# Kernel optimization log

Measured on AMD Instinct MI355X. Metric: run time of the kernel, lower is better.

## Reference

```python
import jax, jax.numpy as jnp
import numpy as np

B, N, E = 8, 512, 65536          # graphs per batch, nodes per graph, total edges
D_IN, D_H = 128, 64              # psi_1 in/out channels
R_IN, R_OUT = 32, 32             # psi_2 in/out channels (rnd indicator dim)
STEPS = 2                        # num consensus steps
NT = B * N                       # total nodes


def _gnn(x, src, dst, ea, W_root, W_nbr, b):
    """Edge-weighted GraphConv: relu(x W_root + A_w x W_nbr + b)."""
    msg = x[src] * ea                                    # [E, F] gather + scale
    agg = jax.ops.segment_sum(msg, dst, num_segments=NT)  # scatter-add
    return jax.nn.relu(x @ W_root + agg @ W_nbr + b)


def setup_inputs() -> dict:
    key = jax.random.key(0)
    ks = jax.random.split(key, 16)
    off = jnp.repeat(jnp.arange(B, dtype=jnp.int32) * N, E // B)  # keep edges within graphs

    def edges(k):
        k1, k2 = jax.random.split(k)
        src = jax.random.randint(k1, (E,), 0, N) + off
        dst = jax.random.randint(k2, (E,), 0, N) + off
        return jnp.stack([src, dst]).astype(jnp.int32)

    s = 0.1
    inp = {
        "x_s": jax.random.normal(ks[0], (NT, D_IN), jnp.float32),
        "edge_index_s": edges(ks[1]),
        "edge_attr_s": jax.random.uniform(ks[2], (E, 1), jnp.float32),
        "batch_s": jnp.repeat(jnp.arange(B, dtype=jnp.int32), N),
        "x_t": jax.random.normal(ks[3], (NT, D_IN), jnp.float32),
        "edge_index_t": edges(ks[4]),
        "edge_attr_t": jax.random.uniform(ks[5], (E, 1), jnp.float32),
        "batch_t": jnp.repeat(jnp.arange(B, dtype=jnp.int32), N),
        "r_s_all": jax.random.normal(ks[6], (STEPS, B, N, R_IN), jnp.float32),
        # psi_1 params
        "W1_root": jax.random.normal(ks[7], (D_IN, D_H), jnp.float32) * s,
        "W1_nbr": jax.random.normal(ks[8], (D_IN, D_H), jnp.float32) * s,
        "b1": jnp.zeros((D_H,), jnp.float32),
        # psi_2 params
        "W2_root": jax.random.normal(ks[9], (R_IN, R_OUT), jnp.float32) * s,
        "W2_nbr": jax.random.normal(ks[10], (R_IN, R_OUT), jnp.float32) * s,
        "b2": jnp.zeros((R_OUT,), jnp.float32),
        # consensus MLP: Lin(R_OUT,R_OUT) -> ReLU -> Lin(R_OUT,1)
        "Wm1": jax.random.normal(ks[11], (R_OUT, R_OUT), jnp.float32) * s,
        "bm1": jnp.zeros((R_OUT,), jnp.float32),
        "Wm2": jax.random.normal(ks[12], (R_OUT, 1), jnp.float32) * s,
        "bm2": jnp.zeros((1,), jnp.float32),
    }
    return inp


def reference(x_s, edge_index_s, edge_attr_s, batch_s,
              x_t, edge_index_t, edge_attr_t, batch_t, r_s_all,
              W1_root, W1_nbr, b1, W2_root, W2_nbr, b2,
              Wm1, bm1, Wm2, bm2):
    src_s, dst_s = edge_index_s[0], edge_index_s[1]
    src_t, dst_t = edge_index_t[0], edge_index_t[1]

    # psi_1: local matching embeddings
    h_s = _gnn(x_s, src_s, dst_s, edge_attr_s, W1_root, W1_nbr, b1)
    h_t = _gnn(x_t, src_t, dst_t, edge_attr_t, W1_root, W1_nbr, b1)

    # to_dense_batch: graphs are equal-sized (batch = repeat(arange(B), N)),
    # so dense batching is a reshape and all node masks are True ->
    # masked_softmax reduces to plain softmax (masked_fill is a no-op).
    h_s = h_s.reshape(B, N, D_H)
    h_t = h_t.reshape(B, N, D_H)

    S_hat0 = jnp.einsum('bsd,btd->bst', h_s, h_t)  # [B, N, N]
    S_0 = jax.nn.softmax(S_hat0, axis=-1)

    def mlp(D):  # D: [B, N, N, R_OUT] -> [B, N, N]
        h = jax.nn.relu(D @ Wm1 + bm1)
        return (h @ Wm2 + bm2)[..., 0]

    def step(S_hat, r_s):
        S = jax.nn.softmax(S_hat, axis=-1)
        r_t = jnp.einsum('bst,bsr->btr', S, r_s)        # S^T @ r_s
        o_s = _gnn(r_s.reshape(NT, R_IN), src_s, dst_s, edge_attr_s,
                   W2_root, W2_nbr, b2).reshape(B, N, R_OUT)
        o_t = _gnn(r_t.reshape(NT, R_IN), src_t, dst_t, edge_attr_t,
                   W2_root, W2_nbr, b2).reshape(B, N, R_OUT)
        D = o_s[:, :, None, :] - o_t[:, None, :, :]     # [B, N, N, R_OUT]
        return S_hat + mlp(D), None

    S_hat, _ = jax.lax.scan(step, S_hat0, r_s_all)
    S_L = jax.nn.softmax(S_hat, axis=-1)
    return (S_0, S_L)
```

## Files before the change

### kernel.cpp

```cpp
#include <hip/hip_runtime.h>

constexpr int B = 8, N = 512, E = 65536;
constexpr int D_IN = 128, D_H = 64, R_IN = 32, R_OUT = 32;
constexpr int NT = B * N;
constexpr size_t NN = (size_t)B * N * N;
constexpr int CAP = 64;

__global__ __launch_bounds__(256) void setup_pack(
    const int* __restrict__ src_s, const int* __restrict__ dst_s,
    const float* __restrict__ ea_s,
    const int* __restrict__ src_t, const int* __restrict__ dst_t,
    const float* __restrict__ ea_t,
    int* __restrict__ deg, int2* __restrict__ pack_s, int2* __restrict__ pack_t,
    const float* __restrict__ x_s, const float* __restrict__ x_t,
    const float* __restrict__ Wr, const float* __restrict__ Wn,
    const float* __restrict__ b,
    float* __restrict__ xr, float* __restrict__ xn) {
  __shared__ float smem[32 * D_IN + D_IN * 128];
  const int bid = blockIdx.x;
  const int tid = threadIdx.x;

  if (bid < 512) {
    const int gid = bid * 256 + tid;
    const int side = gid >> 16;
    const int e = gid & (E - 1);
    const int* __restrict__ src = side ? src_t : src_s;
    const int* __restrict__ dst = side ? dst_t : dst_s;
    const float* __restrict__ ea = side ? ea_t : ea_s;
    int2* __restrict__ pack = side ? pack_t : pack_s;
    const int d = dst[e];
    const int slot = atomicAdd(&deg[side * NT + d], 1);
    if (slot < CAP)
      pack[((size_t)d << 6) + slot] = make_int2(src[e], __float_as_int(ea[e]));
    return;
  }

  float (*xls)[D_IN] = (float(*)[D_IN])smem;
  float (*Wb)[128]   = (float(*)[128])(smem + 32 * D_IN);
  const int pb = bid - 512;
  const int side = pb >> 7;
  const int n0 = (pb & 127) * 32;
  const float* __restrict__ x = side ? x_t : x_s;

#pragma unroll
  for (int j = 0; j < 4; ++j) {
    const int i = tid + j * 256;
    const int n = i >> 5, k4 = (i & 31) * 4;
    *(float4*)&xls[n][k4] = *(const float4*)(x + (size_t)(n0 + n) * D_IN + k4);
  }
#pragma unroll
  for (int j = 0; j < 8; ++j) {
    const int i = tid + j * 256;
    const int k = i >> 4, c4 = (i & 15) * 4;
    *(float4*)&Wb[k][c4]      = *(const float4*)(Wr + k * D_H + c4);
    *(float4*)&Wb[k][64 + c4] = *(const float4*)(Wn + k * D_H + c4);
  }
  __syncthreads();

  const int c0 = (tid & 31) * 4;
  const int nb = (tid >> 5) * 4;
  float4 bv = make_float4(0.f, 0.f, 0.f, 0.f);
  if (c0 < 64) bv = *(const float4*)(b + c0);
  float4 acc0 = bv, acc1 = bv, acc2 = bv, acc3 = bv;

#pragma unroll 16
  for (int k = 0; k < D_IN; ++k) {
    const float4 w = *(const float4*)&Wb[k][c0];
    const float x0 = xls[nb + 0][k];
    const float x1 = xls[nb + 1][k];
    const float x2 = xls[nb + 2][k];
    const float x3 = xls[nb + 3][k];
    acc0.x += x0 * w.x; acc0.y += x0 * w.y; acc0.z += x0 * w.z; acc0.w += x0 * w.w;
    acc1.x += x1 * w.x; acc1.y += x1 * w.y; acc1.z += x1 * w.z; acc1.w += x1 * w.w;
    acc2.x += x2 * w.x; acc2.y += x2 * w.y; acc2.z += x2 * w.z; acc2.w += x2 * w.w;
    acc3.x += x3 * w.x; acc3.y += x3 * w.y; acc3.z += x3 * w.z; acc3.w += x3 * w.w;
  }

  const size_t gbase = (size_t)(side * NT + n0 + nb);
  if (c0 < 64) {
    *(float4*)(xr + (gbase + 0) * D_H + c0) = acc0;
    *(float4*)(xr + (gbase + 1) * D_H + c0) = acc1;
    *(float4*)(xr + (gbase + 2) * D_H + c0) = acc2;
    *(float4*)(xr + (gbase + 3) * D_H + c0) = acc3;
  } else {
    const int c = c0 - 64;
    *(float4*)(xn + (gbase + 0) * D_H + c) = acc0;
    *(float4*)(xn + (gbase + 1) * D_H + c) = acc1;
    *(float4*)(xn + (gbase + 2) * D_H + c) = acc2;
    *(float4*)(xn + (gbase + 3) * D_H + c) = acc3;
  }
}

__global__ __launch_bounds__(256) void agg_pack(
    const float* __restrict__ xn, const float* __restrict__ xr,
    const int* __restrict__ deg,
    const int2* __restrict__ pack_s, const int2* __restrict__ pack_t,
    float* __restrict__ h,
    const float* __restrict__ r_all,
    const float* __restrict__ W2r, const float* __restrict__ W2n,
    const float* __restrict__ b2,
    const float* __restrict__ Wm1, const float* __restrict__ bm1,
    float* __restrict__ Psb) {
  __shared__ float sh[3 * 8 * 33];
  const int bid = blockIdx.x;
  const int tid = threadIdx.x;

  if (bid < 512) {
    const int gid = bid * 256 + tid;
    const int side = gid >> 16;
    const int local = gid & 65535;
    const int n = local >> 4;
    const int c4 = (local & 15) * 4;
    const int2* __restrict__ pack = side ? pack_t : pack_s;
    const float* __restrict__ xb = xn + (size_t)side * NT * D_H;
    const int cnt = deg[side * NT + n];
    const size_t base = (size_t)n << 6;
    float4 acc = make_float4(0.f, 0.f, 0.f, 0.f);
    for (int k = 0; k < cnt; ++k) {
      const int2 p = pack[base + k];
      const float w = __int_as_float(p.y);
      const float4 v = *(const float4*)(xb + (size_t)p.x * D_H + c4);
      acc.x += v.x * w; acc.y += v.y * w; acc.z += v.z * w; acc.w += v.w * w;
    }
    const size_t oi = ((size_t)side * NT + n) * D_H + c4;
    const float4 rv = *(const float4*)(xr + oi);
    *(float4*)(h + oi) = make_float4(fmaxf(rv.x + acc.x, 0.f), fmaxf(rv.y + acc.y, 0.f),
                                     fmaxf(rv.z + acc.z, 0.f), fmaxf(rv.w + acc.w, 0.f));
    return;
  }

  float (*agg)[33] = (float(*)[33])sh;
  float (*rr)[33]  = (float(*)[33])(sh + 8 * 33);
  float (*o)[33]   = (float(*)[33])(sh + 16 * 33);
  const int blk = bid - 512;
  const int st = blk >> 9;
  const int n0 = (blk & 511) * 8;
  const float* __restrict__ r = r_all + (size_t)st * NT * R_IN;
  const int g = tid >> 5, j = tid & 31;
  const int n = n0 + g;
  const int cnt = deg[n];
  const size_t base = (size_t)n << 6;
  float acc = 0.f;
  for (int k = 0; k < cnt; ++k) {
    const int2 p = pack_s[base + k];
    acc += r[(size_t)p.x * R_IN + j] * __int_as_float(p.y);
  }
  agg[g][j] = acc;
  rr[g][j] = r[(size_t)n * R_IN + j];
  __syncthreads();
  float v = b2[j];
#pragma unroll 8
  for (int k = 0; k < 32; ++k)
    v += rr[g][k] * W2r[k * 32 + j] + agg[g][k] * W2n[k * 32 + j];
  o[g][j] = fmaxf(v, 0.f);
  __syncthreads();
  float p2 = bm1[j];
#pragma unroll 8
  for (int k = 0; k < 32; ++k) p2 += o[g][k] * Wm1[k * 32 + j];
  Psb[((size_t)st * NT + n) * 32 + j] = p2;
}

__global__ __launch_bounds__(512) void gemm_sm(const float* __restrict__ h,
                                               float* __restrict__ Shat,
                                               float* __restrict__ S0) {
  __shared__ float hs[16][65];
  __shared__ float ht[256][65];
  const int b = blockIdx.x >> 5;
  const int s0 = (blockIdx.x & 31) * 16;
  const int tid = threadIdx.x;
  const int sg = tid >> 6;
  const int tg = tid & 63;
  const float* __restrict__ h_t = h + (size_t)NT * D_H;

  if (tid < 256) {
    const int r = tid >> 4, c4 = (tid & 15) * 4;
    *(float4*)&hs[r][c4] =
        *(const float4*)(h + ((size_t)(b * N + s0 + r)) * D_H + c4);
  }

  float l[2][4][2];
#pragma unroll
  for (int ch = 0; ch < 2; ++ch) {
    __syncthreads();
#pragma unroll
    for (int jj = 0; jj < 8; ++jj) {
      const int i = tid + jj * 512;
      const int r = i >> 4, c4 = (i & 15) * 4;
      *(float4*)&ht[r][c4] =
          *(const float4*)(h_t + ((size_t)(b * N + ch * 256 + r)) * D_H + c4);
    }
    __syncthreads();
    float a[4][2];
#pragma unroll
    for (int j = 0; j < 4; ++j) { a[j][0] = 0.f; a[j][1] = 0.f; }
#pragma unroll 8
    for (int k = 0; k < D_H; ++k) {
      const float t0v = ht[tg][k];
      const float t1v = ht[tg + 64][k];
      const float t2v = ht[tg + 128][k];
      const float t3v = ht[tg + 192][k];
      const float h0 = hs[sg * 2 + 0][k];
      const float h1 = hs[sg * 2 + 1][k];
      a[0][0] += h0 * t0v; a[0][1] += h1 * t0v;
      a[1][0] += h0 * t1v; a[1][1] += h1 * t1v;
      a[2][0] += h0 * t2v; a[2][1] += h1 * t2v;
      a[3][0] += h0 * t3v; a[3][1] += h1 * t3v;
    }
#pragma unroll
    for (int j = 0; j < 4; ++j) {
      l[ch][j][0] = a[j][0];
      l[ch][j][1] = a[j][1];
    }
  }

  float m[2], inv[2];
#pragma unroll
  for (int i = 0; i < 2; ++i) {
    float mm = -3.4e38f;
#pragma unroll
    for (int ch = 0; ch < 2; ++ch)
#pragma unroll
      for (int j = 0; j < 4; ++j) mm = fmaxf(mm, l[ch][j][i]);
#pragma unroll
    for (int o = 32; o; o >>= 1) mm = fmaxf(mm, __shfl_xor(mm, o));
    m[i] = mm;
  }
#pragma unroll
  for (int i = 0; i < 2; ++i) {
    float ss = 0.f;
#pragma unroll
    for (int ch = 0; ch < 2; ++ch)
#pragma unroll
      for (int j = 0; j < 4; ++j) ss += __expf(l[ch][j][i] - m[i]);
#pragma unroll
    for (int o = 32; o; o >>= 1) ss += __shfl_xor(ss, o);
    inv[i] = 1.0f / ss;
  }
#pragma unroll
  for (int i = 0; i < 2; ++i) {
    const size_t rowb = ((size_t)b * N + s0 + sg * 2 + i) * N;
#pragma unroll
    for (int ch = 0; ch < 2; ++ch)
#pragma unroll
      for (int j = 0; j < 4; ++j) {
        const int t = ch * 256 + j * 64 + tg;
        const float lv = l[ch][j][i];
        Shat[rowb + t] = lv;
        S0[rowb + t] = __expf(lv - m[i]) * inv[i];
      }
  }
}

template <int STATS>
__global__ void rt_part_k(const float* __restrict__ Sdata,
                          const float* __restrict__ rowM, const float* __restrict__ rowInv,
                          const float* __restrict__ rs, float* __restrict__ part) {
  __shared__ float Ss[32][33];
  __shared__ float Rs[32][32];
  const int b = blockIdx.z;
  const int sq = blockIdx.y;
  const int t0 = blockIdx.x * 32;
  const float* Sb = Sdata + (size_t)b * N * N;
  const float* rb = rs + (size_t)b * N * R_IN;
  const int tid = threadIdx.x;
  const int lt = tid >> 3;
  const int r0 = (tid & 7) * 4;
  float a0 = 0, a1 = 0, a2 = 0, a3 = 0;
  for (int c = 0; c < 2; ++c) {
    const int s0 = sq * 64 + c * 32;
    for (int i = tid; i < 1024; i += 256) {
      const int ss = i >> 5, cc = i & 31;
      float v = Sb[(size_t)(s0 + ss) * N + t0 + cc];
      if (STATS) {
        const int grow = b * N + s0 + ss;
        v = __expf(v - rowM[grow]) * rowInv[grow];
      }
      Ss[ss][cc] = v;
      Rs[ss][cc] = rb[(size_t)(s0 + ss) * R_IN + cc];
    }
    __syncthreads();
#pragma unroll 8
    for (int ss = 0; ss < 32; ++ss) {
      const float sv = Ss[ss][lt];
      a0 += sv * Rs[ss][r0 + 0];
      a1 += sv * Rs[ss][r0 + 1];
      a2 += sv * Rs[ss][r0 + 2];
      a3 += sv * Rs[ss][r0 + 3];
    }
    __syncthreads();
  }
  float4* out = (float4*)(part + ((size_t)sq * NT + b * N + t0 + lt) * R_IN + r0);
  *out = make_float4(a0, a1, a2, a3);
}

__global__ void rt_reduce8(const float* __restrict__ part, float* __restrict__ rt) {
  const size_t i = ((size_t)blockIdx.x * 256 + threadIdx.x) * 4;
  float4 a = *(const float4*)(part + i);
#pragma unroll
  for (int p = 1; p < 8; ++p) {
    const float4 v = *(const float4*)(part + (size_t)p * NT * R_IN + i);
    a.x += v.x; a.y += v.y; a.z += v.z; a.w += v.w;
  }
  *(float4*)(rt + i) = a;
}

__global__ __launch_bounds__(256) void gp2t(
    const float* __restrict__ rt_b,
    const int* __restrict__ degp, const int2* __restrict__ pack,
    const float* __restrict__ W2r, const float* __restrict__ W2n,
    const float* __restrict__ b2,
    const float* __restrict__ Wm1, const float* __restrict__ bm1,
    float* __restrict__ Pout) {
  __shared__ float rtb[512][32];
  __shared__ int2 pck[512];
  __shared__ float ag[8][33], rr[8][33], o[8][33];
  const int n0 = blockIdx.x * 8;
  const int bb = n0 >> 9;
  const int tid = threadIdx.x;

  for (int i = tid; i < 4096; i += 256) {
    const int row = i >> 3, k4 = (i & 7) * 4;
    *(float4*)&rtb[row][k4] =
        *(const float4*)(rt_b + ((size_t)(bb * N) + row) * R_IN + k4);
  }
  for (int i = tid; i < 512; i += 256) pck[i] = pack[(size_t)n0 * CAP + i];
  __syncthreads();

  const int g = tid >> 5, j = tid & 31;
  const int n = n0 + g;
  const int cnt = degp[n];
  float acc = 0.f;
  for (int k = 0; k < cnt; ++k) {
    const int2 p = pck[g * CAP + k];
    acc += rtb[p.x & 511][j] * __int_as_float(p.y);
  }
  ag[g][j] = acc;
  rr[g][j] = rtb[n & 511][j];
  __syncthreads();
  float v = b2[j];
#pragma unroll 8
  for (int k = 0; k < 32; ++k)
    v += rr[g][k] * W2r[k * 32 + j] + ag[g][k] * W2n[k * 32 + j];
  o[g][j] = fmaxf(v, 0.f);
  __syncthreads();
  float p2 = 0.f;
#pragma unroll 8
  for (int k = 0; k < 32; ++k) p2 += o[g][k] * Wm1[k * 32 + j];
  Pout[(size_t)n * 32 + j] = p2;
}

template <int LAST>
__global__ void update_sm2(const float* __restrict__ Ps, const float* __restrict__ Pt,
                           const float* __restrict__ Wm2, const float* __restrict__ bm2,
                           float* __restrict__ Shat, float* __restrict__ S,
                           float* __restrict__ rowM, float* __restrict__ rowInv) {
  __shared__ float pt4[128][36];
  const int row0 = blockIdx.x * 8;
  const int b = row0 >> 9;
  const int tid = threadIdx.x;
  const int s_loc = tid >> 5;
  const int lane_t = tid & 31;
  const int row = row0 + s_loc;

  float ps[32], w2v[32];
#pragma unroll
  for (int q = 0; q < 8; ++q) {
    const float4 v = *(const float4*)(Ps + (size_t)row * 32 + q * 4);
    ps[q * 4 + 0] = v.x; ps[q * 4 + 1] = v.y; ps[q * 4 + 2] = v.z; ps[q * 4 + 3] = v.w;
    const float4 w = *(const float4*)(Wm2 + q * 4);
    w2v[q * 4 + 0] = w.x; w2v[q * 4 + 1] = w.y; w2v[q * 4 + 2] = w.z; w2v[q * 4 + 3] = w.w;
  }
  const float bb = bm2[0];

  float l[16];
#pragma unroll
  for (int c = 0; c < 4; ++c) {
    __syncthreads();
#pragma unroll
    for (int j = 0; j < 4; ++j) {
      const int i = tid + j * 256;
      const int t = i >> 3, k4 = (i & 7) * 4;
      const float4 v = *(const float4*)(Pt + ((size_t)(b * N) + c * 128 + t) * 32 + k4);
      *(float4*)&pt4[t][k4] = v;
    }
    __syncthreads();
#pragma unroll
    for (int q = 0; q < 4; ++q) {
      const int tq = q * 32 + lane_t;
      float d = 0.f;
#pragma unroll
      for (int k4 = 0; k4 < 8; ++k4) {
        const float4 pv = *(const float4*)&pt4[tq][k4 * 4];
        d += fmaxf(ps[k4 * 4 + 0] - pv.x, 0.f) * w2v[k4 * 4 + 0];
        d += fmaxf(ps[k4 * 4 + 1] - pv.y, 0.f) * w2v[k4 * 4 + 1];
        d += fmaxf(ps[k4 * 4 + 2] - pv.z, 0.f) * w2v[k4 * 4 + 2];
        d += fmaxf(ps[k4 * 4 + 3] - pv.w, 0.f) * w2v[k4 * 4 + 3];
      }
      const int t = c * 128 + q * 32 + lane_t;
      l[c * 4 + q] = Shat[(size_t)row * N + t] + d + bb;
    }
  }

  float m = l[0];
#pragma unroll
  for (int i = 1; i < 16; ++i) m = fmaxf(m, l[i]);
#pragma unroll
  for (int o = 16; o; o >>= 1) m = fmaxf(m, __shfl_xor(m, o));
  float sum = 0.f;
#pragma unroll
  for (int i = 0; i < 16; ++i) sum += __expf(l[i] - m);
#pragma unroll
  for (int o = 16; o; o >>= 1) sum += __shfl_xor(sum, o);
  const float inv = 1.0f / sum;

  if (!LAST) {
#pragma unroll
    for (int c = 0; c < 4; ++c)
#pragma unroll
      for (int q = 0; q < 4; ++q) {
        const int t = c * 128 + q * 32 + lane_t;
        Shat[(size_t)row * N + t] = l[c * 4 + q];
      }
    if (lane_t == 0) { rowM[row] = m; rowInv[row] = inv; }
  } else {
#pragma unroll
    for (int c = 0; c < 4; ++c)
#pragma unroll
      for (int q = 0; q < 4; ++q) {
        const int t = c * 128 + q * 32 + lane_t;
        S[(size_t)row * N + t] = __expf(l[c * 4 + q] - m) * inv;
      }
  }
}

extern "C" void kernel_launch(void* const* d_in, const int* in_sizes, int n_in,
                              void* d_out, int out_size, void* d_ws, size_t ws_size,
                              hipStream_t stream) {
  const float* x_s  = (const float*)d_in[0];
  const int*   ei_s = (const int*)d_in[1];
  const float* ea_s = (const float*)d_in[2];
  const float* x_t  = (const float*)d_in[4];
  const int*   ei_t = (const int*)d_in[5];
  const float* ea_t = (const float*)d_in[6];
  const float* r_all = (const float*)d_in[8];
  const float* W1r = (const float*)d_in[9];
  const float* W1n = (const float*)d_in[10];
  const float* b1  = (const float*)d_in[11];
  const float* W2r = (const float*)d_in[12];
  const float* W2n = (const float*)d_in[13];
  const float* b2  = (const float*)d_in[14];
  const float* Wm1 = (const float*)d_in[15];
  const float* bm1 = (const float*)d_in[16];
  const float* Wm2 = (const float*)d_in[17];
  const float* bm2 = (const float*)d_in[18];

  const int* src_s = ei_s;
  const int* dst_s = ei_s + E;
  const int* src_t = ei_t;
  const int* dst_t = ei_t + E;

  float* ws = (float*)d_ws;
  float* xr   = ws; ws += (size_t)2 * NT * D_H;
  float* xn   = ws; ws += (size_t)2 * NT * D_H;
  float* h    = ws; ws += (size_t)2 * NT * D_H;
  float* Shat = ws; ws += NN;
  float* rt_p = ws; ws += (size_t)8 * NT * R_IN;
  float* rt_b = ws; ws += (size_t)NT * R_IN;
  float* Psb  = ws; ws += (size_t)2 * NT * R_OUT;
  float* Ptb  = ws; ws += (size_t)NT * R_OUT;
  float* rowM = ws; ws += NT;
  float* rowI = ws; ws += NT;
  int* deg      = (int*)ws; ws += 2 * NT;
  int2* pack_s  = (int2*)ws; ws += (size_t)NT * CAP * 2;
  int2* pack_t  = (int2*)ws; ws += (size_t)NT * CAP * 2;

  float* S0_out = (float*)d_out;
  float* SL_out = S0_out + NN;

  hipMemsetAsync(deg, 0, 2 * NT * sizeof(int), stream);
  setup_pack<<<768, 256, 0, stream>>>(src_s, dst_s, ea_s, src_t, dst_t, ea_t,
                                      deg, pack_s, pack_t,
                                      x_s, x_t, W1r, W1n, b1, xr, xn);
  agg_pack<<<1536, 256, 0, stream>>>(xn, xr, deg, pack_s, pack_t, h,
                                     r_all, W2r, W2n, b2, Wm1, bm1, Psb);
  gemm_sm<<<256, 512, 0, stream>>>(h, Shat, S0_out);

  rt_part_k<0><<<dim3(16, 8, B), 256, 0, stream>>>(S0_out, nullptr, nullptr, r_all, rt_p);
  rt_reduce8<<<128, 256, 0, stream>>>(rt_p, rt_b);
  gp2t<<<512, 256, 0, stream>>>(rt_b, deg + NT, pack_t, W2r, W2n, b2, Wm1, bm1, Ptb);
  update_sm2<0><<<512, 256, 0, stream>>>(Psb, Ptb, Wm2, bm2, Shat, nullptr, rowM, rowI);

  rt_part_k<1><<<dim3(16, 8, B), 256, 0, stream>>>(Shat, rowM, rowI,
                                                   r_all + (size_t)NT * R_IN, rt_p);
  rt_reduce8<<<128, 256, 0, stream>>>(rt_p, rt_b);
  gp2t<<<512, 256, 0, stream>>>(rt_b, deg + NT, pack_t, W2r, W2n, b2, Wm1, bm1, Ptb);
  update_sm2<1><<<512, 256, 0, stream>>>(Psb + (size_t)NT * R_OUT, Ptb, Wm2, bm2,
                                         Shat, SL_out, nullptr, nullptr);
}
```

Before: 200.3 us.

## Transpose x tile in LDS, vectorize gemm_sm reads, widen update_sm2 blocks

setup_pack now stores the x tile transposed with padding so the inner GEMM loop reads neighbouring node values instead of strided rows. gemm_sm pads rows to 68 floats and reads float4 from LDS, cutting LDS instruction count. update_sm2 moves from 256-thread blocks of 8 rows to 512-thread blocks of 16 rows, halving Pt tile loads per row. The transposed scalar stores in setup_pack and the 68-float row stride may introduce LDS bank conflicts, and the larger update blocks reduce block count.

Measured after the change: 212.2 us. 5.9% more time.

```diff
diff --git a/kernel.cpp b/kernel.cpp
--- a/kernel.cpp
+++ b/kernel.cpp
@@ -16,7 +16,8 @@
     const float* __restrict__ Wr, const float* __restrict__ Wn,
     const float* __restrict__ b,
     float* __restrict__ xr, float* __restrict__ xn) {
-  __shared__ float smem[32 * D_IN + D_IN * 128];
+  __shared__ float xT[D_IN][33];
+  __shared__ float Wb[D_IN][128];
   const int bid = blockIdx.x;
   const int tid = threadIdx.x;
 
@@ -35,8 +36,6 @@
     return;
   }
 
-  float (*xls)[D_IN] = (float(*)[D_IN])smem;
-  float (*Wb)[128]   = (float(*)[128])(smem + 32 * D_IN);
   const int pb = bid - 512;
   const int side = pb >> 7;
   const int n0 = (pb & 127) * 32;
@@ -46,7 +45,11 @@
   for (int j = 0; j < 4; ++j) {
     const int i = tid + j * 256;
     const int n = i >> 5, k4 = (i & 31) * 4;
-    *(float4*)&xls[n][k4] = *(const float4*)(x + (size_t)(n0 + n) * D_IN + k4);
+    const float4 v = *(const float4*)(x + (size_t)(n0 + n) * D_IN + k4);
+    xT[k4 + 0][n] = v.x;
+    xT[k4 + 1][n] = v.y;
+    xT[k4 + 2][n] = v.z;
+    xT[k4 + 3][n] = v.w;
   }
 #pragma unroll
   for (int j = 0; j < 8; ++j) {
@@ -66,10 +69,10 @@
 #pragma unroll 16
   for (int k = 0; k < D_IN; ++k) {
     const float4 w = *(const float4*)&Wb[k][c0];
-    const float x0 = xls[nb + 0][k];
-    const float x1 = xls[nb + 1][k];
-    const float x2 = xls[nb + 2][k];
-    const float x3 = xls[nb + 3][k];
+    const float x0 = xT[k][nb + 0];
+    const float x1 = xT[k][nb + 1];
+    const float x2 = xT[k][nb + 2];
+    const float x3 = xT[k][nb + 3];
     acc0.x += x0 * w.x; acc0.y += x0 * w.y; acc0.z += x0 * w.z; acc0.w += x0 * w.w;
     acc1.x += x1 * w.x; acc1.y += x1 * w.y; acc1.z += x1 * w.z; acc1.w += x1 * w.w;
     acc2.x += x2 * w.x; acc2.y += x2 * w.y; acc2.z += x2 * w.z; acc2.w += x2 * w.w;
@@ -163,8 +166,8 @@
 __global__ __launch_bounds__(512) void gemm_sm(const float* __restrict__ h,
                                                float* __restrict__ Shat,
                                                float* __restrict__ S0) {
-  __shared__ float hs[16][65];
-  __shared__ float ht[256][65];
+  __shared__ float hs[16][68];
+  __shared__ float ht[256][68];
   const int b = blockIdx.x >> 5;
   const int s0 = (blockIdx.x & 31) * 16;
   const int tid = threadIdx.x;
@@ -193,18 +196,22 @@
     float a[4][2];
 #pragma unroll
     for (int j = 0; j < 4; ++j) { a[j][0] = 0.f; a[j][1] = 0.f; }
-#pragma unroll 8
-    for (int k = 0; k < D_H; ++k) {
-      const float t0v = ht[tg][k];
-      const float t1v = ht[tg + 64][k];
-      const float t2v = ht[tg + 128][k];
-      const float t3v = ht[tg + 192][k];
-      const float h0 = hs[sg * 2 + 0][k];
-      const float h1 = hs[sg * 2 + 1][k];
-      a[0][0] += h0 * t0v; a[0][1] += h1 * t0v;
-      a[1][0] += h0 * t1v; a[1][1] += h1 * t1v;
-      a[2][0] += h0 * t2v; a[2][1] += h1 * t2v;
-      a[3][0] += h0 * t3v; a[3][1] += h1 * t3v;
+#pragma unroll
+    for (int k = 0; k < D_H; k += 4) {
+      const float4 h0 = *(const float4*)&hs[sg * 2 + 0][k];
+      const float4 h1 = *(const float4*)&hs[sg * 2 + 1][k];
+      const float4 t0 = *(const float4*)&ht[tg][k];
+      const float4 t1 = *(const float4*)&ht[tg + 64][k];
+      const float4 t2 = *(const float4*)&ht[tg + 128][k];
+      const float4 t3 = *(const float4*)&ht[tg + 192][k];
+      a[0][0] += h0.x * t0.x + h0.y * t0.y + h0.z * t0.z + h0.w * t0.w;
+      a[0][1] += h1.x * t0.x + h1.y * t0.y + h1.z * t0.z + h1.w * t0.w;
+      a[1][0] += h0.x * t1.x + h0.y * t1.y + h0.z * t1.z + h0.w * t1.w;
+      a[1][1] += h1.x * t1.x + h1.y * t1.y + h1.z * t1.z + h1.w * t1.w;
+      a[2][0] += h0.x * t2.x + h0.y * t2.y + h0.z * t2.z + h0.w * t2.w;
+      a[2][1] += h1.x * t2.x + h1.y * t2.y + h1.z * t2.z + h1.w * t2.w;
+      a[3][0] += h0.x * t3.x + h0.y * t3.y + h0.z * t3.z + h0.w * t3.w;
+      a[3][1] += h1.x * t3.x + h1.y * t3.y + h1.z * t3.z + h1.w * t3.w;
     }
 #pragma unroll
     for (int j = 0; j < 4; ++j) {
@@ -350,12 +357,13 @@
 }
 
 template <int LAST>
-__global__ void update_sm2(const float* __restrict__ Ps, const float* __restrict__ Pt,
-                           const float* __restrict__ Wm2, const float* __restrict__ bm2,
-                           float* __restrict__ Shat, float* __restrict__ S,
-                           float* __restrict__ rowM, float* __restrict__ rowInv) {
+__global__ __launch_bounds__(512) void update_sm2(
+    const float* __restrict__ Ps, const float* __restrict__ Pt,
+    const float* __restrict__ Wm2, const float* __restrict__ bm2,
+    float* __restrict__ Shat, float* __restrict__ S,
+    float* __restrict__ rowM, float* __restrict__ rowInv) {
   __shared__ float pt4[128][36];
-  const int row0 = blockIdx.x * 8;
+  const int row0 = blockIdx.x * 16;
   const int b = row0 >> 9;
   const int tid = threadIdx.x;
   const int s_loc = tid >> 5;
@@ -377,8 +385,8 @@
   for (int c = 0; c < 4; ++c) {
     __syncthreads();
 #pragma unroll
-    for (int j = 0; j < 4; ++j) {
-      const int i = tid + j * 256;
+    for (int j = 0; j < 2; ++j) {
+      const int i = tid + j * 512;
       const int t = i >> 3, k4 = (i & 7) * 4;
       const float4 v = *(const float4*)(Pt + ((size_t)(b * N) + c * 128 + t) * 32 + k4);
       *(float4*)&pt4[t][k4] = v;
@@ -488,12 +496,12 @@
   rt_part_k<0><<<dim3(16, 8, B), 256, 0, stream>>>(S0_out, nullptr, nullptr, r_all, rt_p);
   rt_reduce8<<<128, 256, 0, stream>>>(rt_p, rt_b);
   gp2t<<<512, 256, 0, stream>>>(rt_b, deg + NT, pack_t, W2r, W2n, b2, Wm1, bm1, Ptb);
-  update_sm2<0><<<512, 256, 0, stream>>>(Psb, Ptb, Wm2, bm2, Shat, nullptr, rowM, rowI);
+  update_sm2<0><<<256, 512, 0, stream>>>(Psb, Ptb, Wm2, bm2, Shat, nullptr, rowM, rowI);
 
   rt_part_k<1><<<dim3(16, 8, B), 256, 0, stream>>>(Shat, rowM, rowI,
                                                    r_all + (size_t)NT * R_IN, rt_p);
   rt_reduce8<<<128, 256, 0, stream>>>(rt_p, rt_b);
   gp2t<<<512, 256, 0, stream>>>(rt_b, deg + NT, pack_t, W2r, W2n, b2, Wm1, bm1, Ptb);
-  update_sm2<1><<<512, 256, 0, stream>>>(Psb + (size_t)NT * R_OUT, Ptb, Wm2, bm2,
+  update_sm2<1><<<256, 512, 0, stream>>>(Psb + (size_t)NT * R_OUT, Ptb, Wm2, bm2,
                                          Shat, SL_out, nullptr, nullptr);
 }
```
